# Kernel optimization log

Measured on AMD Instinct MI355X. Metric: run time of the kernel, lower is better.

Reference implementation:

```python
import jax, jax.numpy as jnp
import numpy as np

N = 200_000   # total nodes across batched AIGs
E = 400_000   # edges (fan-in ~2 per gate)
D = 64        # input_dim == dim_hidden (required by in-place scatter in _gru_forward)
B = 16        # number of graphs in batch
LF = 12       # num forward topological levels
LB = 12       # num backward topological levels
NUM_ROUNDS = 1


def setup_inputs() -> dict:
    key = jax.random.key(0)
    ks = jax.random.split(key, 9)
    node_type = jax.random.randint(ks[0], (N,), 0, 3, dtype=jnp.int32)
    num_inverted_predecessors = jax.random.randint(ks[1], (N,), 0, 3, dtype=jnp.int32)
    edge_index = jax.random.randint(ks[2], (2, E), 0, N, dtype=jnp.int32)
    forward_level = jax.random.randint(ks[3], (N,), 0, LF, dtype=jnp.int32)
    backward_level = jax.random.randint(ks[4], (N,), 0, LB, dtype=jnp.int32)
    batch = jnp.sort(jax.random.randint(ks[5], (N,), 0, B, dtype=jnp.int32))
    s = 1.0 / np.sqrt(D)
    W_enc = jax.random.normal(ks[6], (2, D), dtype=jnp.float32) * 0.5
    b_enc = jnp.zeros((D,), dtype=jnp.float32)
    W_f = jax.random.normal(ks[7], (D, D), dtype=jnp.float32) * s
    b_f = jnp.zeros((D,), dtype=jnp.float32)
    W_b = jax.random.normal(ks[8], (D, D), dtype=jnp.float32) * s
    b_b = jnp.zeros((D,), dtype=jnp.float32)
    return dict(node_type=node_type,
                num_inverted_predecessors=num_inverted_predecessors,
                edge_index=edge_index,
                forward_level=forward_level,
                backward_level=backward_level,
                batch=batch,
                W_enc=W_enc, b_enc=b_enc,
                W_f=W_f, b_f=b_f,
                W_b=W_b, b_b=b_b)


def reference(node_type, num_inverted_predecessors, edge_index,
              forward_level, backward_level, batch,
              W_enc, b_enc, W_f, b_f, W_b, b_b):
    # h_init = node_encoder(cat(node_type, num_inverted_predecessors))
    x = jnp.stack([node_type, num_inverted_predecessors], axis=1).astype(W_enc.dtype)  # [N,2]
    h = x @ W_enc + b_enc  # [N,D] node_state
    src, dst = edge_index[0], edge_index[1]

    for _ in range(NUM_ROUNDS):
        # forward topological sweep: level l nodes receive sum of mlp(h_src)
        # over incoming edges whose destination is at level l (subgraph dim=1).
        for l in range(1, LF):
            m = h @ W_f + b_f                                    # AggConv mlp on current state
            e_w = (forward_level[dst] == l).astype(h.dtype)      # edges into level-l nodes
            msg = jax.ops.segment_sum(m[src] * e_w[:, None], dst, num_segments=N)
            h = jnp.where((forward_level == l)[:, None], msg, h)  # scatter l_msg into node_state
        # backward sweep (reverse flow): level-l sources receive sum of
        # mlp_b(h_dst) over outgoing edges (subgraph dim=0, target_to_source).
        for l in range(1, LB):
            m = h @ W_b + b_b
            e_w = (backward_level[src] == l).astype(h.dtype)
            msg = jax.ops.segment_sum(m[dst] * e_w[:, None], src, num_segments=N)
            h = jnp.where((backward_level == l)[:, None], msg, h)

    # readout over output nodes (node_type == 1): [global_max_pool, global_add_pool]
    out_mask = (node_type == 1)
    neg_inf = jnp.finfo(h.dtype).min
    max_pool = jax.ops.segment_max(jnp.where(out_mask[:, None], h, neg_inf), batch, num_segments=B)
    sum_pool = jax.ops.segment_sum(h * out_mask[:, None].astype(h.dtype), batch, num_segments=B)
    return jnp.concatenate([max_pool, sum_pool], axis=1)  # [B, 2*D]
```

## Files before the change

kernel.cpp:

```cpp
#include <hip/hip_runtime.h>
#include <float.h>

#define NLVL 12
#define NB   16


struct Params {
    const int *nt, *ninv, *src, *dst, *fl, *bl, *batch;
    const float *We, *be, *Wf, *bf, *Wb, *bb;
    float *hN, *hB, *tabg, *out;
    int *rowptr, *cursor, *col, *nb_f, *nb_b, *onodes, *bsums, *meta, *plarr;
    int N, E, M, outN;
};

__device__ __forceinline__ float rlanef(float x, int l) {
    return __int_as_float(__builtin_amdgcn_readlane(__float_as_int(x), l));
}

__global__ void k_deg_hist(Params p) {
    __shared__ int hf[NLVL], hb[NLVL], ho[NB];
    if (threadIdx.x < NLVL) { hf[threadIdx.x] = 0; hb[threadIdx.x] = 0; }
    if (threadIdx.x < NB) ho[threadIdx.x] = 0;
    __syncthreads();
    int g = blockIdx.x * blockDim.x + threadIdx.x, gs = gridDim.x * blockDim.x;
    for (int e = g; e < p.E; e += gs) {
        atomicAdd(&p.rowptr[p.dst[e]], 1);
        atomicAdd(&p.rowptr[p.N + p.src[e]], 1);
    }
    for (int i = g; i < p.N; i += gs) {
        int f = p.fl[i], b = p.bl[i];
        int t = p.nt[i], iv = p.ninv[i];
        p.plarr[i] = f | (b << 4) | ((t * 3 + iv) << 8);
        atomicAdd(&hf[f], 1);
        atomicAdd(&hb[b], 1);
        if (t == 1) atomicAdd(&ho[p.batch[i]], 1);
    }
    __syncthreads();
    if (threadIdx.x < NLVL) { atomicAdd(&p.meta[threadIdx.x], hf[threadIdx.x]); atomicAdd(&p.meta[16 + threadIdx.x], hb[threadIdx.x]); }
    if (threadIdx.x < NB) atomicAdd(&p.meta[32 + threadIdx.x], ho[threadIdx.x]);
}

__global__ void k_scan1(int* __restrict__ data, int M, int* __restrict__ bsums) {
    __shared__ int s[512];
    int t = threadIdx.x;
    int g = blockIdx.x * 512 + t;
    int v = (g < M) ? data[g] : 0;
    s[t] = v;
    __syncthreads();
    for (int off = 1; off < 512; off <<= 1) {
        int add = (t >= off) ? s[t - off] : 0;
        __syncthreads();
        s[t] += add;
        __syncthreads();
    }
    if (g < M) data[g] = s[t] - v;
    if (t == 511) bsums[blockIdx.x] = s[511];
}

__global__ void k_scan_top(int* __restrict__ bsums, int nblk, Params p,
                           float* __restrict__ out, int outN) {
    __shared__ int s[1024];
    int* meta = p.meta;
    int t = threadIdx.x;
    if (t == 0) { int a = 0; for (int l = 0; l < NLVL; l++) { meta[96 + l] = a; meta[48 + l] = a; a += meta[l]; } meta[96 + NLVL] = a; }
    if (t == 1) { int a = 0; for (int l = 0; l < NLVL; l++) { meta[128 + l] = a; meta[64 + l] = a; a += meta[16 + l]; } meta[128 + NLVL] = a; }
    if (t == 2) { int a = 0; for (int b = 0; b < NB; b++) { meta[160 + b] = a; meta[80 + b] = a; a += meta[32 + b]; } meta[160 + NB] = a; }
    for (int i = t; i < outN; i += 1024)
        out[i] = ((i & 127) < 64) ? -FLT_MAX : 0.0f;
    if (t < 576) {
        int row = t >> 6, j = t & 63;
        float nf = (float)(row / 3), iv = (float)(row % 3);
        p.tabg[t] = fmaf(nf, p.We[j], fmaf(iv, p.We[64 + j], p.be[j]));
    }
    int v = (t < nblk) ? bsums[t] : 0;
    s[t] = v;
    __syncthreads();
    for (int off = 1; off < 1024; off <<= 1) {
        int add = (t >= off) ? s[t - off] : 0;
        __syncthreads();
        s[t] += add;
        __syncthreads();
    }
    if (t < nblk) bsums[t] = s[t] - v;
}

__global__ void k_scan_add(int* __restrict__ rowptr, int* __restrict__ cursor, int M, int total,
                           const int* __restrict__ bsums) {
    int g = blockIdx.x * blockDim.x + threadIdx.x;
    if (g >= M) return;
    int r = rowptr[g] + bsums[g >> 9];
    rowptr[g] = r;
    cursor[g] = r;
    if (g == 0) rowptr[M] = total;
}

__global__ void k_fill(Params p) {
    __shared__ int hf[NLVL], hb[NLVL], ho[NB], basef[NLVL], baseb[NLVL], baseo[NB];
    int g = blockIdx.x * blockDim.x + threadIdx.x, gs = gridDim.x * blockDim.x;
    int tid = threadIdx.x;
    int N = p.N;

    for (int e = g; e < p.E; e += gs) {
        int s = p.src[e], d = p.dst[e];
        p.col[atomicAdd(&p.cursor[d], 1)] = s | (p.plarr[s] << 18);
        p.col[atomicAdd(&p.cursor[N + s], 1)] = d | (p.plarr[d] << 18);
    }

    for (int i0 = blockIdx.x * blockDim.x; i0 < N; i0 += gs) {
        int i = i0 + tid;
        bool valid = (i < N);
        if (tid < NLVL) { hf[tid] = 0; hb[tid] = 0; }
        if (tid < NB) ho[tid] = 0;
        __syncthreads();
        int lf = 0, lb = 0, ob = -1, pl = 0;
        if (valid) {
            pl = p.plarr[i];
            lf = pl & 15; lb = (pl >> 4) & 15;
            atomicAdd(&hf[lf], 1);
            atomicAdd(&hb[lb], 1);
            if (p.nt[i] == 1) { ob = p.batch[i]; atomicAdd(&ho[ob], 1); }
        }
        __syncthreads();
        if (tid < NLVL) {
            basef[tid] = atomicAdd(&p.meta[48 + tid], hf[tid]);
            baseb[tid] = atomicAdd(&p.meta[64 + tid], hb[tid]);
            hf[tid] = 0; hb[tid] = 0;
        }
        if (tid < NB) {
            baseo[tid] = atomicAdd(&p.meta[80 + tid], ho[tid]);
            ho[tid] = 0;
        }
        __syncthreads();
        if (valid) {
            int pk = i | (pl << 18);
            p.nb_f[basef[lf] + atomicAdd(&hf[lf], 1)] = pk;
            p.nb_b[baseb[lb] + atomicAdd(&hb[lb], 1)] = pk;
            if (ob >= 0) p.onodes[baseo[ob] + atomicAdd(&ho[ob], 1)] = pk;
        }
        __syncthreads();
    }
}

__global__ __launch_bounds__(256, 4) void k_sweep(Params p, int lvl, int dir) {
    const int tid = threadIdx.x, lane = tid & 63;
    const float* W = dir ? p.Wb : p.Wf;
    float w[64];
    #pragma unroll
    for (int k = 0; k < 64; k++) w[k] = W[k * 64 + lane];
    float bv = (dir ? p.bb : p.bf)[lane];

    const int* nb = dir ? p.nb_b : p.nb_f;
    const int* rp = p.rowptr + (dir ? p.N : 0);
    int start = p.meta[(dir ? 128 : 96) + lvl];
    int cnt   = p.meta[(dir ? 128 : 96) + lvl + 1] - start;
    const int wid = (blockIdx.x * 256 + tid) >> 6;
    const int nw  = (gridDim.x * 256) >> 6;
    const int q = lane >> 4, fb = (lane & 15) * 4;
    float* db = dir ? p.hB : p.hN;

    int c0 = (int)((long long)cnt * wid / nw);
    int c1 = (int)((long long)cnt * (wid + 1) / nw);
    for (int i = c0; i < c1; i += 4) {
        int my = i + q;
        int v = 0, rpv = 0, rpe = 0;
        if (my < c1) {
            int e = nb[start + my];
            v = e & 0x3FFFF;
            rpv = rp[v]; rpe = rp[v + 1];
        }
        float4 acc = make_float4(0.f, 0.f, 0.f, 0.f);
        for (int cb = rpv; cb < rpe; cb++) {
            int cu = p.col[cb];
            int u = cu & 0x3FFFF;
            int flu = (cu >> 18) & 15, blu = (cu >> 22) & 15;
            const float* sp;
            if (dir == 0)
                sp = (flu > 0 && flu < lvl) ? (p.hN + (size_t)u * 64)
                                            : (p.tabg + ((cu >> 26) & 15) * 64);
            else
                sp = (blu > 0 && blu < lvl) ? (p.hB + (size_t)u * 64)
                   : (flu > 0)              ? (p.hN + (size_t)u * 64)
                                            : (p.tabg + ((cu >> 26) & 15) * 64);
            const float4 x = *(const float4*)(sp + fb);
            acc.x += x.x; acc.y += x.y; acc.z += x.z; acc.w += x.w;
        }
        #pragma unroll
        for (int qq = 0; qq < 4; qq++) {
            if (i + qq >= c1) break;
            int vs   = __builtin_amdgcn_readlane(v, 16 * qq);
            int degs = __builtin_amdgcn_readlane(rpe, 16 * qq)
                     - __builtin_amdgcn_readlane(rpv, 16 * qq);
            float o = bv * (float)degs;
            #pragma unroll
            for (int m = 0; m < 16; m++) {
                float ax = rlanef(acc.x, 16 * qq + m);
                float ay = rlanef(acc.y, 16 * qq + m);
                float az = rlanef(acc.z, 16 * qq + m);
                float aw = rlanef(acc.w, 16 * qq + m);
                o = fmaf(ax, w[4 * m + 0], o);
                o = fmaf(ay, w[4 * m + 1], o);
                o = fmaf(az, w[4 * m + 2], o);
                o = fmaf(aw, w[4 * m + 3], o);
            }
            db[(size_t)vs * 64 + lane] = o;
        }
    }
}

__device__ inline void atomicMaxF(float* addr, float val) {
    int* ai = (int*)addr;
    int old = *ai;
    while (__int_as_float(old) < val) {
        int assumed = old;
        old = atomicCAS(ai, assumed, __float_as_int(val));
        if (old == assumed) break;
    }
}

__global__ void k_readout(Params p) {
    int lane = threadIdx.x & 63;
    int b = blockIdx.x >> 5;
    int sl = blockIdx.x & 31;
    int a0 = p.meta[160 + b], a1 = p.meta[161 + b];
    int cnt = a1 - a0;
    if (cnt == 0) return;
    int lo = a0 + (int)((long long)cnt * sl / 32);
    int hi = a0 + (int)((long long)cnt * (sl + 1) / 32);
    int wcnt = hi - lo;
    int wave = threadIdx.x >> 6;
    int wl = lo + (wcnt * wave) / 4;
    int wh = lo + (wcnt * (wave + 1)) / 4;
    if (wh <= wl) return;
    float mx = -FLT_MAX, sm = 0.f;
    for (int k = wl; k < wh; k += 64) {
        int take = wh - k; if (take > 64) take = 64;
        int el = (lane < take) ? p.onodes[k + lane] : 0;
        for (int j = 0; j < take; j++) {
            int e = __shfl(el, j, 64);
            int v = e & 0x3FFFF;
            int flv = (e >> 18) & 15, blv = (e >> 22) & 15;
            const float* sp = (blv > 0) ? (p.hB + (size_t)v * 64)
                            : (flv > 0) ? (p.hN + (size_t)v * 64)
                                        : (p.tabg + ((e >> 26) & 15) * 64);
            float x = sp[lane];
            mx = fmaxf(mx, x);
            sm += x;
        }
    }
    atomicMaxF(&p.out[b * 128 + lane], mx);
    atomicAdd(&p.out[b * 128 + 64 + lane], sm);
}

extern "C" void kernel_launch(void* const* d_in, const int* in_sizes, int n_in,
                              void* d_out, int out_size, void* d_ws, size_t ws_size,
                              hipStream_t stream) {
    int N = in_sizes[0];
    int E = in_sizes[2] / 2;
    int M = 2 * N;

    Params p;
    p.nt    = (const int*)d_in[0];
    p.ninv  = (const int*)d_in[1];
    p.src   = (const int*)d_in[2];
    p.dst   = (const int*)d_in[2] + E;
    p.fl    = (const int*)d_in[3];
    p.bl    = (const int*)d_in[4];
    p.batch = (const int*)d_in[5];
    p.We    = (const float*)d_in[6];
    p.be    = (const float*)d_in[7];
    p.Wf    = (const float*)d_in[8];
    p.bf    = (const float*)d_in[9];
    p.Wb    = (const float*)d_in[10];
    p.bb    = (const float*)d_in[11];
    p.out   = (float*)d_out;
    p.N = N; p.E = E; p.M = M; p.outN = out_size;

    char* ws = (char*)d_ws;
    size_t off = 0;
    auto alloc = [&](size_t bytes) -> char* {
        char* q = ws + off;
        off = (off + bytes + 255) & ~(size_t)255;
        return q;
    };
    p.rowptr = (int*)  alloc((size_t)(M + 1) * sizeof(int));
    p.meta   = (int*)  alloc(256 * sizeof(int));
    size_t zbytes = (size_t)((char*)(p.meta + 256) - (char*)p.rowptr);
    p.hN     = (float*)alloc((size_t)N * 64 * sizeof(float));
    p.hB     = (float*)alloc((size_t)N * 64 * sizeof(float));
    p.tabg   = (float*)alloc(9 * 64 * sizeof(float));
    p.cursor = (int*)  alloc((size_t)M * sizeof(int));
    p.col    = (int*)  alloc((size_t)2 * E * sizeof(int));
    p.nb_f   = (int*)  alloc((size_t)N * sizeof(int));
    p.nb_b   = (int*)  alloc((size_t)N * sizeof(int));
    p.onodes = (int*)  alloc((size_t)N * sizeof(int));
    p.plarr  = (int*)  alloc((size_t)N * sizeof(int));
    p.bsums  = (int*)  alloc(1024 * sizeof(int));

    int nscan = (M + 511) / 512;

    hipMemsetAsync(p.rowptr, 0, zbytes, stream);
    k_deg_hist<<<1024, 256, 0, stream>>>(p);
    k_scan1<<<nscan, 512, 0, stream>>>(p.rowptr, M, p.bsums);
    k_scan_top<<<1, 1024, 0, stream>>>(p.bsums, nscan, p, p.out, out_size);
    k_scan_add<<<(M + 255) / 256, 256, 0, stream>>>(p.rowptr, p.cursor, M, 2 * E, p.bsums);
    k_fill<<<1024, 256, 0, stream>>>(p);

    for (int l = 1; l < NLVL; l++)
        k_sweep<<<1024, 256, 0, stream>>>(p, l, 0);
    for (int l = 1; l < NLVL; l++)
        k_sweep<<<1024, 256, 0, stream>>>(p, l, 1);

    k_readout<<<NB * 32, 256, 0, stream>>>(p);
}
```

Measured before the change: 485.6 us.

## Replace global-atomic level bucketing with per-block counts and prefix-scanned offsets

Result: no change. 478.0 us, median of 2 (-1.6%).

```diff
diff --git a/kernel.cpp b/kernel.cpp
--- a/kernel.cpp
+++ b/kernel.cpp
@@ -3,6 +3,7 @@
 
 #define NLVL 12
 #define NB   16
+#define NBLK 256
 
 
 struct Params {
@@ -10,6 +11,7 @@
     const float *We, *be, *Wf, *bf, *Wb, *bb;
     float *hN, *hB, *tabg, *out;
     int *rowptr, *cursor, *col, *nb_f, *nb_b, *onodes, *bsums, *meta, *plarr;
+    int *cntf, *cntb, *cnto, *blkf, *blkb, *blko;
     int N, E, M, outN;
 };
 
@@ -19,15 +21,18 @@
 
 __global__ void k_deg_hist(Params p) {
     __shared__ int hf[NLVL], hb[NLVL], ho[NB];
-    if (threadIdx.x < NLVL) { hf[threadIdx.x] = 0; hb[threadIdx.x] = 0; }
-    if (threadIdx.x < NB) ho[threadIdx.x] = 0;
-    __syncthreads();
-    int g = blockIdx.x * blockDim.x + threadIdx.x, gs = gridDim.x * blockDim.x;
+    int tid = threadIdx.x, bid = blockIdx.x;
+    if (tid < NLVL) { hf[tid] = 0; hb[tid] = 0; }
+    if (tid < NB) ho[tid] = 0;
+    __syncthreads();
+    int g = bid * 256 + tid, gs = gridDim.x * 256;
     for (int e = g; e < p.E; e += gs) {
         atomicAdd(&p.rowptr[p.dst[e]], 1);
         atomicAdd(&p.rowptr[p.N + p.src[e]], 1);
     }
-    for (int i = g; i < p.N; i += gs) {
+    int chunk = (p.N + gridDim.x - 1) / gridDim.x;
+    int lo = bid * chunk, hi = lo + chunk; if (hi > p.N) hi = p.N;
+    for (int i = lo + tid; i < hi; i += 256) {
         int f = p.fl[i], b = p.bl[i];
         int t = p.nt[i], iv = p.ninv[i];
         p.plarr[i] = f | (b << 4) | ((t * 3 + iv) << 8);
@@ -36,8 +41,8 @@
         if (t == 1) atomicAdd(&ho[p.batch[i]], 1);
     }
     __syncthreads();
-    if (threadIdx.x < NLVL) { atomicAdd(&p.meta[threadIdx.x], hf[threadIdx.x]); atomicAdd(&p.meta[16 + threadIdx.x], hb[threadIdx.x]); }
-    if (threadIdx.x < NB) atomicAdd(&p.meta[32 + threadIdx.x], ho[threadIdx.x]);
+    if (tid < NLVL) { p.cntf[tid * NBLK + bid] = hf[tid]; p.cntb[tid * NBLK + bid] = hb[tid]; }
+    if (tid < NB) p.cnto[tid * NBLK + bid] = ho[tid];
 }
 
 __global__ void k_scan1(int* __restrict__ data, int M, int* __restrict__ bsums) {
@@ -60,11 +65,9 @@
 __global__ void k_scan_top(int* __restrict__ bsums, int nblk, Params p,
                            float* __restrict__ out, int outN) {
     __shared__ int s[1024];
+    __shared__ int tot[48];
+    int t = threadIdx.x;
     int* meta = p.meta;
-    int t = threadIdx.x;
-    if (t == 0) { int a = 0; for (int l = 0; l < NLVL; l++) { meta[96 + l] = a; meta[48 + l] = a; a += meta[l]; } meta[96 + NLVL] = a; }
-    if (t == 1) { int a = 0; for (int l = 0; l < NLVL; l++) { meta[128 + l] = a; meta[64 + l] = a; a += meta[16 + l]; } meta[128 + NLVL] = a; }
-    if (t == 2) { int a = 0; for (int b = 0; b < NB; b++) { meta[160 + b] = a; meta[80 + b] = a; a += meta[32 + b]; } meta[160 + NB] = a; }
     for (int i = t; i < outN; i += 1024)
         out[i] = ((i & 127) < 64) ? -FLT_MAX : 0.0f;
     if (t < 576) {
@@ -72,6 +75,50 @@
         float nf = (float)(row / 3), iv = (float)(row % 3);
         p.tabg[t] = fmaf(nf, p.We[j], fmaf(iv, p.We[64 + j], p.be[j]));
     }
+    int seg = t >> 8, b = t & 255;
+    for (int r = 0; r < 3; r++) {
+        int l = 4 * r + seg;
+        int v = p.cntf[l * NBLK + b];
+        s[t] = v; __syncthreads();
+        for (int off = 1; off < NBLK; off <<= 1) {
+            int add = (b >= off) ? s[t - off] : 0; __syncthreads();
+            s[t] += add; __syncthreads();
+        }
+        p.blkf[l * NBLK + b] = s[t] - v;
+        if (b == NBLK - 1) tot[l] = s[t];
+        __syncthreads();
+    }
+    for (int r = 0; r < 3; r++) {
+        int l = 4 * r + seg;
+        int v = p.cntb[l * NBLK + b];
+        s[t] = v; __syncthreads();
+        for (int off = 1; off < NBLK; off <<= 1) {
+            int add = (b >= off) ? s[t - off] : 0; __syncthreads();
+            s[t] += add; __syncthreads();
+        }
+        p.blkb[l * NBLK + b] = s[t] - v;
+        if (b == NBLK - 1) tot[16 + l] = s[t];
+        __syncthreads();
+    }
+    for (int r = 0; r < 4; r++) {
+        int l = 4 * r + seg;
+        int v = p.cnto[l * NBLK + b];
+        s[t] = v; __syncthreads();
+        for (int off = 1; off < NBLK; off <<= 1) {
+            int add = (b >= off) ? s[t - off] : 0; __syncthreads();
+            s[t] += add; __syncthreads();
+        }
+        p.blko[l * NBLK + b] = s[t] - v;
+        if (b == NBLK - 1) tot[32 + l] = s[t];
+        __syncthreads();
+    }
+    if (t == 0) { int a = 0; for (int l = 0; l < NLVL; l++) { meta[96 + l] = a; a += tot[l]; } meta[96 + NLVL] = a; }
+    if (t == 1) { int a = 0; for (int l = 0; l < NLVL; l++) { meta[128 + l] = a; a += tot[16 + l]; } meta[128 + NLVL] = a; }
+    if (t == 2) { int a = 0; for (int l = 0; l < NB; l++) { meta[160 + l] = a; a += tot[32 + l]; } meta[160 + NB] = a; }
+    __syncthreads();
+    for (int i = t; i < NLVL * NBLK; i += 1024) p.blkf[i] += meta[96 + (i >> 8)];
+    for (int i = t; i < NLVL * NBLK; i += 1024) p.blkb[i] += meta[128 + (i >> 8)];
+    for (int i = t; i < NB * NBLK; i += 1024) p.blko[i] += meta[160 + (i >> 8)];
     int v = (t < nblk) ? bsums[t] : 0;
     s[t] = v;
     __syncthreads();
@@ -95,9 +142,9 @@
 }
 
 __global__ void k_fill(Params p) {
-    __shared__ int hf[NLVL], hb[NLVL], ho[NB], basef[NLVL], baseb[NLVL], baseo[NB];
-    int g = blockIdx.x * blockDim.x + threadIdx.x, gs = gridDim.x * blockDim.x;
-    int tid = threadIdx.x;
+    __shared__ int cur[48];
+    int tid = threadIdx.x, bid = blockIdx.x;
+    int g = bid * 256 + tid, gs = gridDim.x * 256;
     int N = p.N;
 
     for (int e = g; e < p.E; e += gs) {
@@ -106,38 +153,19 @@
         p.col[atomicAdd(&p.cursor[N + s], 1)] = d | (p.plarr[d] << 18);
     }
 
-    for (int i0 = blockIdx.x * blockDim.x; i0 < N; i0 += gs) {
-        int i = i0 + tid;
-        bool valid = (i < N);
-        if (tid < NLVL) { hf[tid] = 0; hb[tid] = 0; }
-        if (tid < NB) ho[tid] = 0;
-        __syncthreads();
-        int lf = 0, lb = 0, ob = -1, pl = 0;
-        if (valid) {
-            pl = p.plarr[i];
-            lf = pl & 15; lb = (pl >> 4) & 15;
-            atomicAdd(&hf[lf], 1);
-            atomicAdd(&hb[lb], 1);
-            if (p.nt[i] == 1) { ob = p.batch[i]; atomicAdd(&ho[ob], 1); }
-        }
-        __syncthreads();
-        if (tid < NLVL) {
-            basef[tid] = atomicAdd(&p.meta[48 + tid], hf[tid]);
-            baseb[tid] = atomicAdd(&p.meta[64 + tid], hb[tid]);
-            hf[tid] = 0; hb[tid] = 0;
-        }
-        if (tid < NB) {
-            baseo[tid] = atomicAdd(&p.meta[80 + tid], ho[tid]);
-            ho[tid] = 0;
-        }
-        __syncthreads();
-        if (valid) {
-            int pk = i | (pl << 18);
-            p.nb_f[basef[lf] + atomicAdd(&hf[lf], 1)] = pk;
-            p.nb_b[baseb[lb] + atomicAdd(&hb[lb], 1)] = pk;
-            if (ob >= 0) p.onodes[baseo[ob] + atomicAdd(&ho[ob], 1)] = pk;
-        }
-        __syncthreads();
+    if (tid < NLVL) { cur[tid] = p.blkf[tid * NBLK + bid]; cur[16 + tid] = p.blkb[tid * NBLK + bid]; }
+    if (tid < NB) cur[32 + tid] = p.blko[tid * NBLK + bid];
+    __syncthreads();
+    int chunk = (N + gridDim.x - 1) / gridDim.x;
+    int lo = bid * chunk, hi = lo + chunk; if (hi > N) hi = N;
+    for (int i = lo + tid; i < hi; i += 256) {
+        int pl = p.plarr[i];
+        int lf = pl & 15, lb = (pl >> 4) & 15, tx = (pl >> 8) & 15;
+        int pk = i | (pl << 18);
+        p.nb_f[atomicAdd(&cur[lf], 1)] = pk;
+        p.nb_b[atomicAdd(&cur[16 + lb], 1)] = pk;
+        if (tx >= 3 && tx < 6)
+            p.onodes[atomicAdd(&cur[32 + p.batch[i]], 1)] = pk;
     }
 }
 
@@ -295,15 +323,21 @@
     p.onodes = (int*)  alloc((size_t)N * sizeof(int));
     p.plarr  = (int*)  alloc((size_t)N * sizeof(int));
     p.bsums  = (int*)  alloc(1024 * sizeof(int));
+    p.cntf   = (int*)  alloc(NLVL * NBLK * sizeof(int));
+    p.cntb   = (int*)  alloc(NLVL * NBLK * sizeof(int));
+    p.cnto   = (int*)  alloc(NB * NBLK * sizeof(int));
+    p.blkf   = (int*)  alloc(NLVL * NBLK * sizeof(int));
+    p.blkb   = (int*)  alloc(NLVL * NBLK * sizeof(int));
+    p.blko   = (int*)  alloc(NB * NBLK * sizeof(int));
 
     int nscan = (M + 511) / 512;
 
     hipMemsetAsync(p.rowptr, 0, zbytes, stream);
-    k_deg_hist<<<1024, 256, 0, stream>>>(p);
+    k_deg_hist<<<NBLK, 256, 0, stream>>>(p);
     k_scan1<<<nscan, 512, 0, stream>>>(p.rowptr, M, p.bsums);
     k_scan_top<<<1, 1024, 0, stream>>>(p.bsums, nscan, p, p.out, out_size);
     k_scan_add<<<(M + 255) / 256, 256, 0, stream>>>(p.rowptr, p.cursor, M, 2 * E, p.bsums);
-    k_fill<<<1024, 256, 0, stream>>>(p);
+    k_fill<<<NBLK, 256, 0, stream>>>(p);
 
     for (int l = 1; l < NLVL; l++)
         k_sweep<<<1024, 256, 0, stream>>>(p, l, 0);
```
